# Performance work log

Measured on AMD Instinct MI355X. Metric: run time of the kernel, lower is better.

Reference implementation:

```python
import jax, jax.numpy as jnp
import numpy as np

N, B, NUM_NODES, D_IN = 16384, 16, 1024, 1024
H, C = 4, 128
E = 262144


def _g(k, shape, fan_in):
    return jax.random.normal(k, shape, jnp.float32) * (1.0 / np.sqrt(fan_in))


def setup_inputs() -> dict:
    key = jax.random.key(0)
    ks = jax.random.split(key, 32)
    HC = H * C
    inp = {
        'x': jax.random.normal(ks[0], (N, D_IN), jnp.float32),
        'edge_index': jax.random.randint(ks[1], (2, E), 0, N, dtype=jnp.int64),
        'batch': jnp.repeat(jnp.arange(B, dtype=jnp.int64), NUM_NODES),
        # GATConv 1 (D_IN -> H x C, concat)
        'W1': _g(ks[2], (D_IN, HC), D_IN),
        'att_src1': _g(ks[3], (H, C), C),
        'att_dst1': _g(ks[4], (H, C), C),
        'b1': jnp.zeros((HC,), jnp.float32),
        # GATConv 2 (H*C -> H x C, concat)
        'W2': _g(ks[5], (HC, HC), HC),
        'att_src2': _g(ks[6], (H, C), C),
        'att_dst2': _g(ks[7], (H, C), C),
        'b2': jnp.zeros((HC,), jnp.float32),
        # pooling linears (HC -> 1)
        'p1w': _g(ks[8], (HC, 1), HC), 'p1b': jnp.zeros((1,), jnp.float32),
        'p2w': _g(ks[9], (HC, 1), HC), 'p2b': jnp.zeros((1,), jnp.float32),
        # layer_norm0 (applied to x2 per original code)
        'ln_g': jnp.ones((NUM_NODES,), jnp.float32),
        'ln_b': jnp.zeros((NUM_NODES,), jnp.float32),
        # encoder MLP 1024->512->256->128->64, last 64->1
        'fw1': _g(ks[10], (NUM_NODES, 512), NUM_NODES), 'fb1': jnp.zeros((512,), jnp.float32),
        'fw2': _g(ks[11], (512, 256), 512), 'fb2': jnp.zeros((256,), jnp.float32),
        'fw3': _g(ks[12], (256, 128), 256), 'fb3': jnp.zeros((128,), jnp.float32),
        'fw4': _g(ks[13], (128, 64), 128), 'fb4': jnp.zeros((64,), jnp.float32),
        'lw': _g(ks[14], (64, 1), 64), 'lb': jnp.zeros((1,), jnp.float32),
    }
    return inp


def gat_conv(x, src, dst, W, a_src, a_dst, b):
    # x: [N, F_in] -> h: [N, H, C]
    h = (x @ W).reshape(N, H, C)
    alpha_src = jnp.sum(h * a_src[None], axis=-1)  # [N, H]
    alpha_dst = jnp.sum(h * a_dst[None], axis=-1)  # [N, H]
    e = jax.nn.leaky_relu(alpha_src[src] + alpha_dst[dst], 0.2)  # [E', H]
    # segment softmax over destination neighborhoods (every node has a self loop)
    emax = jax.ops.segment_max(e, dst, num_segments=N)
    ex = jnp.exp(e - emax[dst])
    denom = jax.ops.segment_sum(ex, dst, num_segments=N)
    alpha = ex / (denom[dst] + 1e-16)  # [E', H]
    msg = h[src] * alpha[:, :, None]  # [E', H, C]
    out = jax.ops.segment_sum(msg, dst, num_segments=N)  # [N, H, C]
    return out.reshape(N, H * C) + b


def layer_norm(x, g, b, eps=1e-5):
    mu = jnp.mean(x, axis=-1, keepdims=True)
    var = jnp.var(x, axis=-1, keepdims=True)
    return (x - mu) * jax.lax.rsqrt(var + eps) * g + b


def reference(x, edge_index, batch, W1, att_src1, att_dst1, b1, W2, att_src2, att_dst2, b2,
              p1w, p1b, p2w, p2b, ln_g, ln_b, fw1, fb1, fw2, fb2, fw3, fb3, fw4, fb4, lw, lb):
    # add self loops (GATConv default)
    loops = jnp.arange(N, dtype=edge_index.dtype)
    src = jnp.concatenate([edge_index[0], loops])
    dst = jnp.concatenate([edge_index[1], loops])

    h1 = jax.nn.elu(gat_conv(x, src, dst, W1, att_src1, att_dst1, b1))
    # pool1 + to_dense_batch: batch is sorted with NUM_NODES nodes per graph -> reshape
    x1 = (h1 @ p1w + p1b).squeeze(-1).reshape(B, NUM_NODES)
    h2 = jax.nn.elu(gat_conv(h1, src, dst, W2, att_src2, att_dst2, b2))
    x2 = (h2 @ p2w + p2b).squeeze(-1).reshape(B, NUM_NODES)

    # opt.layer_norm=True; original bug: x2 normalized by layer_norm0
    x2 = layer_norm(x2, ln_g, ln_b)
    multiscale = x2  # which_layer == 'layer3'

    e = jax.nn.elu(multiscale @ fw1 + fb1)
    e = jax.nn.elu(e @ fw2 + fb2)
    e = jax.nn.elu(e @ fw3 + fb3)
    e = jax.nn.elu(e @ fw4 + fb4)
    pred = e @ lw + lb  # act_type='none' -> no activation
    return multiscale, e, pred
```

## Files before the change

kernel.cpp:

```cpp
#include <hip/hip_runtime.h>
#include <math.h>

#define NN    16384
#define DIN   1024
#define HCdim 512
#define NHEAD 4
#define NE_   262144
#define EP_   (NE_ + NN)

using short8  = __attribute__((ext_vector_type(8))) short;
using floatx4 = __attribute__((ext_vector_type(4))) float;

typedef __attribute__((address_space(3))) unsigned int lds_uint;
typedef const __attribute__((address_space(1))) unsigned int glb_uint;
#define ASYNC_LD16(g, l) __builtin_amdgcn_global_load_lds((glb_uint*)(g), (lds_uint*)(l), 16, 0, 0)

__device__ __forceinline__ float eluf(float x){ return x > 0.f ? x : expm1f(x); }
__device__ __forceinline__ float lrelu(float x){ return x > 0.f ? x : 0.2f * x; }
__device__ __forceinline__ float bf2f(unsigned short u){
    union { unsigned int i; float f; } c; c.i = ((unsigned int)u) << 16; return c.f;
}
__device__ __forceinline__ unsigned short f2b(float f){
    union { float f; unsigned int u; } c; c.f = f;
    unsigned int u = c.u;
    return (unsigned short)((u + 0x7FFFu + ((u >> 16) & 1u)) >> 16);
}

__global__ void k_zero_i(int* __restrict__ p, int n){
    int i = blockIdx.x * 256 + threadIdx.x;
    if (i < n) p[i] = 0;
}

__global__ void k_degree(const int* __restrict__ ei, int* __restrict__ deg){
    int i = blockIdx.x * 256 + threadIdx.x;
    if (i >= EP_) return;
    int d = (i < NE_) ? ei[NE_ + i] : (i - NE_);
    atomicAdd(&deg[d], 1);
}

__global__ __launch_bounds__(1024) void k_scan(const int* __restrict__ deg, int* __restrict__ offs){
    __shared__ int s[1024];
    int tid  = threadIdx.x;
    int base = tid * 16;
    int local[16];
    int sum = 0;
    #pragma unroll
    for (int i = 0; i < 16; i++){ local[i] = deg[base + i]; sum += local[i]; }
    s[tid] = sum;
    __syncthreads();
    for (int off = 1; off < 1024; off <<= 1){
        int v = (tid >= off) ? s[tid - off] : 0;
        __syncthreads();
        s[tid] += v;
        __syncthreads();
    }
    int run = (tid == 0) ? 0 : s[tid - 1];
    #pragma unroll
    for (int i = 0; i < 16; i++){ offs[base + i] = run; run += local[i]; }
    if (tid == 1023) offs[NN] = run;
}

__global__ void k_scatter(const int* __restrict__ ei, const int* __restrict__ offs,
                          int* __restrict__ cursor, int* __restrict__ csr){
    int i = blockIdx.x * 256 + threadIdx.x;
    if (i >= EP_) return;
    int srcv, dstv;
    if (i < NE_){ srcv = ei[i]; dstv = ei[NE_ + i]; }
    else        { srcv = dstv = i - NE_; }
    int pos = offs[dstv] + atomicAdd(&cursor[dstv], 1);
    csr[pos] = srcv;
}

__global__ __launch_bounds__(256) void k_casts(const float* __restrict__ x, ushort* __restrict__ xb,
    const float* __restrict__ W1, ushort* __restrict__ W1T,
    const float* __restrict__ W2, ushort* __restrict__ W2T){
    int bid = blockIdx.x, tid = threadIdx.x;
    if (bid < 16384){
        int i = bid * 256 + tid;
        float4 v = *(const float4*)(x + (size_t)i * 4);
        ushort4 o = { f2b(v.x), f2b(v.y), f2b(v.z), f2b(v.w) };
        *(ushort4*)(xb + (size_t)i * 4) = o;
    } else if (bid < 16384 + 512){
        int t = (bid - 16384) * 256 + tid;
        int n = t >> 8, kb = (t & 255) * 4;
        ushort4 o = { f2b(W1[(size_t)(kb+0)*HCdim + n]), f2b(W1[(size_t)(kb+1)*HCdim + n]),
                      f2b(W1[(size_t)(kb+2)*HCdim + n]), f2b(W1[(size_t)(kb+3)*HCdim + n]) };
        *(ushort4*)(W1T + (size_t)n * DIN + kb) = o;
    } else {
        int t = (bid - 16896) * 256 + tid;
        int n = t >> 7, kb = (t & 127) * 4;
        ushort4 o = { f2b(W2[(size_t)(kb+0)*HCdim + n]), f2b(W2[(size_t)(kb+1)*HCdim + n]),
                      f2b(W2[(size_t)(kb+2)*HCdim + n]), f2b(W2[(size_t)(kb+3)*HCdim + n]) };
        *(ushort4*)(W2T + (size_t)n * HCdim + kb) = o;
    }
}

__global__ __launch_bounds__(256) void gemm_bf16(const ushort* __restrict__ A,
                                                 const ushort* __restrict__ BT,
                                                 signed char* __restrict__ C,
                                                 const float* __restrict__ att_s,
                                                 const float* __restrict__ att_d,
                                                 float* __restrict__ as_, float* __restrict__ ad_,
                                                 float* __restrict__ sclb,
                                                 int M, int Nn, int K){
    __shared__ ushort As[2][64 * 32];
    __shared__ ushort Bs[2][128 * 32];
    __shared__ float prS[2][64];
    __shared__ float prD[2][64];
    __shared__ float amx[2][64];
    int tid = threadIdx.x;
    int m0 = blockIdx.x * 64, n0 = blockIdx.y * 128;
    int cx = blockIdx.y;
    int lane = tid & 63, w = tid >> 6;
    int wm = (w >> 1) * 32, wn = (w & 1) * 64;
    int la = lane & 15, qd = lane >> 4;

    int srow = tid >> 2, schunk = (tid & 3) * 8;
    const ushort* Ag = A  + (size_t)(m0 + srow) * K + schunk;
    const ushort* Bg = BT + (size_t)(n0 + srow) * K + schunk;
    ushort* Asw0 = &As[0][srow * 32 + schunk];
    ushort* Asw1 = &As[1][srow * 32 + schunk];
    ushort* Bsw0 = &Bs[0][srow * 32 + schunk];
    ushort* Bsw1 = &Bs[1][srow * 32 + schunk];

    floatx4 acc[4][2] = {};
    for (int k0 = 0; k0 < K; k0 += 64){
        __syncthreads();
        ASYNC_LD16(Ag + k0,                       Asw0);
        ASYNC_LD16(Ag + k0 + 32,                  Asw1);
        ASYNC_LD16(Bg + k0,                       Bsw0);
        ASYNC_LD16(Bg + (size_t)64 * K + k0,      Bsw0 + 64 * 32);
        ASYNC_LD16(Bg + k0 + 32,                  Bsw1);
        ASYNC_LD16(Bg + (size_t)64 * K + k0 + 32, Bsw1 + 64 * 32);
        __syncthreads();
        #pragma unroll
        for (int kk = 0; kk < 2; kk++){
            short8 af[2], bf[4];
            #pragma unroll
            for (int j = 0; j < 2; j++)
                af[j] = *(const short8*)&As[kk][(wm + j*16 + la) * 32 + qd * 8];
            #pragma unroll
            for (int i = 0; i < 4; i++)
                bf[i] = *(const short8*)&Bs[kk][(wn + i*16 + la) * 32 + qd * 8];
            #pragma unroll
            for (int i = 0; i < 4; i++)
                #pragma unroll
                for (int j = 0; j < 2; j++)
                    acc[i][j] = __builtin_amdgcn_mfma_f32_16x16x32_bf16(bf[i], af[j], acc[i][j], 0, 0, 0);
        }
    }
    float4 s4[4], d4[4];
    #pragma unroll
    for (int i = 0; i < 4; i++){
        s4[i] = *(const float4*)(att_s + cx * 128 + wn + i * 16 + qd * 4);
        d4[i] = *(const float4*)(att_d + cx * 128 + wn + i * 16 + qd * 4);
    }
    int half = wn >> 6;
    #pragma unroll
    for (int j = 0; j < 2; j++){
        float ps = 0.f, pd = 0.f;
        #pragma unroll
        for (int i = 0; i < 4; i++){
            ps = fmaf(acc[i][j][0], s4[i].x, ps); pd = fmaf(acc[i][j][0], d4[i].x, pd);
            ps = fmaf(acc[i][j][1], s4[i].y, ps); pd = fmaf(acc[i][j][1], d4[i].y, pd);
            ps = fmaf(acc[i][j][2], s4[i].z, ps); pd = fmaf(acc[i][j][2], d4[i].z, pd);
            ps = fmaf(acc[i][j][3], s4[i].w, ps); pd = fmaf(acc[i][j][3], d4[i].w, pd);
        }
        ps += __shfl_xor(ps, 16); ps += __shfl_xor(ps, 32);
        pd += __shfl_xor(pd, 16); pd += __shfl_xor(pd, 32);
        float am = 0.f;
        #pragma unroll
        for (int i = 0; i < 4; i++){
            am = fmaxf(am, fabsf(acc[i][j][0])); am = fmaxf(am, fabsf(acc[i][j][1]));
            am = fmaxf(am, fabsf(acc[i][j][2])); am = fmaxf(am, fabsf(acc[i][j][3]));
        }
        am = fmaxf(am, __shfl_xor(am, 16)); am = fmaxf(am, __shfl_xor(am, 32));
        if (lane < 16){
            prS[half][wm + j * 16 + la] = ps;
            prD[half][wm + j * 16 + la] = pd;
            amx[half][wm + j * 16 + la] = am;
        }
    }
    __syncthreads();
    #pragma unroll
    for (int j = 0; j < 2; j++){
        int nl = wm + j * 16 + la;
        float amax = fmaxf(fmaxf(amx[0][nl], amx[1][nl]), 1e-20f);
        float inv = 127.0f / amax;
        #pragma unroll
        for (int i = 0; i < 4; i++){
            int q0 = (int)rintf(acc[i][j][0] * inv);
            int q1 = (int)rintf(acc[i][j][1] * inv);
            int q2 = (int)rintf(acc[i][j][2] * inv);
            int q3 = (int)rintf(acc[i][j][3] * inv);
            unsigned pk = (q0 & 0xff) | ((q1 & 0xff) << 8) | ((q2 & 0xff) << 16) | ((q3 & 0xff) << 24);
            *(unsigned*)(C + (size_t)(m0 + nl) * HCdim + n0 + wn + i * 16 + qd * 4) = pk;
        }
    }
    if (tid < 64){
        as_[(size_t)(m0 + tid) * 4 + cx]  = prS[0][tid] + prS[1][tid];
        ad_[(size_t)(m0 + tid) * 4 + cx]  = prD[0][tid] + prD[1][tid];
        sclb[(size_t)(m0 + tid) * 4 + cx] = fmaxf(fmaxf(amx[0][tid], amx[1][tid]), 1e-20f) * (1.f / 127.f);
    }
}

__global__ __launch_bounds__(256) void k_edgew(const int* __restrict__ offs, const int* __restrict__ csr,
    const float* __restrict__ as_, const float* __restrict__ ad_,
    const float* __restrict__ sclb, unsigned* __restrict__ wbuf){
    int wv = threadIdx.x >> 6, lane = threadIdx.x & 63;
    int n = blockIdx.x * 4 + wv;
    int start = offs[n], end = offs[n + 1];
    float4 ad4 = *(const float4*)(ad_ + (size_t)n * 4);
    for (int j = start + lane; j < end; j += 64){
        int s = csr[j];
        float4 as4 = *(const float4*)(as_ + (size_t)s * 4);
        float4 sc4 = *(const float4*)(sclb + (size_t)s * 4);
        float w0 = __expf(lrelu(as4.x + ad4.x));
        float w1 = __expf(lrelu(as4.y + ad4.y));
        float w2 = __expf(lrelu(as4.z + ad4.z));
        float w3 = __expf(lrelu(as4.w + ad4.w));
        uint4 o;
        o.x = (unsigned)f2b(w0) | ((unsigned)f2b(w0 * sc4.x) << 16);
        o.y = (unsigned)f2b(w1) | ((unsigned)f2b(w1 * sc4.y) << 16);
        o.z = (unsigned)f2b(w2) | ((unsigned)f2b(w2 * sc4.z) << 16);
        o.w = (unsigned)f2b(w3) | ((unsigned)f2b(w3 * sc4.w) << 16);
        *(uint4*)(wbuf + (size_t)j * 4) = o;
    }
}

template<bool POOL>
__global__ __launch_bounds__(256) void k_aggregate(const signed char* __restrict__ h,
    const int* __restrict__ offs, const int* __restrict__ csr,
    const unsigned* __restrict__ wbuf,
    const float* __restrict__ bias, ushort* __restrict__ out,
    const float* __restrict__ pw, const float* __restrict__ pb, float* __restrict__ x2){
    int wv   = threadIdx.x >> 6;
    int lane = threadIdx.x & 63;
    int n    = blockIdx.x * 4 + wv;
    int cb   = lane * 8;
    int head = lane >> 4;
    int start = offs[n], end = offs[n + 1];
    const signed char* hrow = h + cb;
    float dsum = 0.f;
    float a0=0.f,a1=0.f,a2=0.f,a3=0.f,a4=0.f,a5=0.f,a6=0.f,a7=0.f;

    for (int base = start; base < end; base += 64){
        int bcnt = min(64, end - base);
        int pre = csr[base + min(lane, bcnt - 1)];
        unsigned wA0, wA1, wA2, wA3, wB0, wB1, wB2, wB3;
        uint2 hA0, hA1, hA2, hA3, hB0, hB1, hB2, hB3;

#define LOADE(W, H, E)                                                        \
        { int e_ = (E); int ec_ = min(e_, bcnt - 1);                          \
          int s_ = __builtin_amdgcn_readlane(pre, ec_);                       \
          unsigned wp_ = wbuf[(size_t)(base + ec_) * 4 + head];               \
          W = (e_ < bcnt) ? wp_ : 0u;                                         \
          H = *(const uint2*)(hrow + (size_t)s_ * HCdim); }

#define CONS(W, H)                                                            \
        { float w_  = bf2f((unsigned short)(W & 0xffff));                     \
          float ws_ = bf2f((unsigned short)(W >> 16));                        \
          dsum += w_;                                                         \
          int q0 = (int)(H.x << 24) >> 24;                                    \
          int q1 = (int)(H.x << 16) >> 24;                                    \
          int q2 = (int)(H.x <<  8) >> 24;                                    \
          int q3 = (int) H.x        >> 24;                                    \
          int q4 = (int)(H.y << 24) >> 24;                                    \
          int q5 = (int)(H.y << 16) >> 24;                                    \
          int q6 = (int)(H.y <<  8) >> 24;                                    \
          int q7 = (int) H.y        >> 24;                                    \
          a0 = fmaf(ws_, (float)q0, a0); a1 = fmaf(ws_, (float)q1, a1);       \
          a2 = fmaf(ws_, (float)q2, a2); a3 = fmaf(ws_, (float)q3, a3);       \
          a4 = fmaf(ws_, (float)q4, a4); a5 = fmaf(ws_, (float)q5, a5);       \
          a6 = fmaf(ws_, (float)q6, a6); a7 = fmaf(ws_, (float)q7, a7); }

        LOADE(wA0, hA0, 0) LOADE(wA1, hA1, 1) LOADE(wA2, hA2, 2) LOADE(wA3, hA3, 3)
        for (int g = 0; g < bcnt; g += 8){
            LOADE(wB0, hB0, g + 4) LOADE(wB1, hB1, g + 5)
            LOADE(wB2, hB2, g + 6) LOADE(wB3, hB3, g + 7)
            CONS(wA0, hA0) CONS(wA1, hA1) CONS(wA2, hA2) CONS(wA3, hA3)
            LOADE(wA0, hA0, g + 8) LOADE(wA1, hA1, g + 9)
            LOADE(wA2, hA2, g + 10) LOADE(wA3, hA3, g + 11)
            CONS(wB0, hB0) CONS(wB1, hB1) CONS(wB2, hB2) CONS(wB3, hB3)
        }
#undef LOADE
#undef CONS
    }
    float rden = 1.f / (dsum + 1e-16f);
    float4 b0 = *(const float4*)(bias + cb);
    float4 b1 = *(const float4*)(bias + cb + 4);
    float e0 = eluf(fmaf(a0, rden, b0.x));
    float e1 = eluf(fmaf(a1, rden, b0.y));
    float e2 = eluf(fmaf(a2, rden, b0.z));
    float e3 = eluf(fmaf(a3, rden, b0.w));
    float e4 = eluf(fmaf(a4, rden, b1.x));
    float e5 = eluf(fmaf(a5, rden, b1.y));
    float e6 = eluf(fmaf(a6, rden, b1.z));
    float e7 = eluf(fmaf(a7, rden, b1.w));
    if (!POOL){
        uint4 o;
        o.x = (unsigned)f2b(e0) | ((unsigned)f2b(e1) << 16);
        o.y = (unsigned)f2b(e2) | ((unsigned)f2b(e3) << 16);
        o.z = (unsigned)f2b(e4) | ((unsigned)f2b(e5) << 16);
        o.w = (unsigned)f2b(e6) | ((unsigned)f2b(e7) << 16);
        *(uint4*)(out + (size_t)n * HCdim + cb) = o;
    } else {
        float4 w0p = *(const float4*)(pw + cb);
        float4 w1p = *(const float4*)(pw + cb + 4);
        float s = e0*w0p.x + e1*w0p.y + e2*w0p.z + e3*w0p.w
                + e4*w1p.x + e5*w1p.y + e6*w1p.z + e7*w1p.w;
        #pragma unroll
        for (int off = 32; off; off >>= 1) s += __shfl_down(s, off);
        if (lane == 0) x2[n] = s + pb[0];
    }
}

__global__ __launch_bounds__(256) void k_fc1_ln(const float* __restrict__ x2,
    const float* __restrict__ lng, const float* __restrict__ lnb,
    const float* __restrict__ W, const float* __restrict__ bias,
    float* __restrict__ outms, float* __restrict__ e1b){
    __shared__ float xs[1024];
    __shared__ float red[4][64];
    __shared__ float red2[8];
    __shared__ float stats[2];
    int tid = threadIdx.x;
    int b = blockIdx.y, c0 = blockIdx.x * 64;
    float4 v = *(const float4*)(x2 + b * 1024 + tid * 4);
    float s  = v.x + v.y + v.z + v.w;
    float sq = v.x * v.x + v.y * v.y + v.z * v.z + v.w * v.w;
    #pragma unroll
    for (int off = 32; off; off >>= 1){ s += __shfl_down(s, off); sq += __shfl_down(sq, off); }
    if ((tid & 63) == 0){ red2[(tid >> 6) * 2] = s; red2[(tid >> 6) * 2 + 1] = sq; }
    __syncthreads();
    if (tid == 0){
        float S  = red2[0] + red2[2] + red2[4] + red2[6];
        float SQ = red2[1] + red2[3] + red2[5] + red2[7];
        float mu  = S * (1.f / 1024.f);
        float var = SQ * (1.f / 1024.f) - mu * mu;
        stats[0] = mu; stats[1] = rsqrtf(var + 1e-5f);
    }
    __syncthreads();
    float mu = stats[0], r = stats[1];
    float4 g4  = *(const float4*)(lng + tid * 4);
    float4 bb4 = *(const float4*)(lnb + tid * 4);
    float4 o;
    o.x = (v.x - mu) * r * g4.x + bb4.x;
    o.y = (v.y - mu) * r * g4.y + bb4.y;
    o.z = (v.z - mu) * r * g4.z + bb4.z;
    o.w = (v.w - mu) * r * g4.w + bb4.w;
    *(float4*)&xs[tid * 4] = o;
    if (blockIdx.x == 0) *(float4*)(outms + b * 1024 + tid * 4) = o;
    __syncthreads();
    int tx = tid & 63, ty = tid >> 6;
    const float* wp = W + (size_t)(ty * 256) * 512 + c0 + tx;
    float a = 0.f;
    #pragma unroll 8
    for (int i = 0; i < 256; i++)
        a = fmaf(xs[ty * 256 + i], wp[(size_t)i * 512], a);
    red[ty][tx] = a;
    __syncthreads();
    if (ty == 0){
        float vv = red[0][tx] + red[1][tx] + red[2][tx] + red[3][tx] + bias[c0 + tx];
        e1b[b * 512 + c0 + tx] = eluf(vv);
    }
}

template<int K, int NOUT>
__global__ __launch_bounds__(256) void k_fc(const float* __restrict__ in,
    const float* __restrict__ W, const float* __restrict__ bias, float* __restrict__ outb){
    __shared__ float xs[K];
    __shared__ float red[4][64];
    int tid = threadIdx.x;
    int b = blockIdx.y, c0 = blockIdx.x * 64;
    int tx = tid & 63, ty = tid >> 6;
    for (int i = tid * 4; i < K; i += 1024)
        *(float4*)&xs[i] = *(const float4*)(in + b * K + i);
    __syncthreads();
    const float* wp = W + (size_t)(ty * (K / 4)) * NOUT + c0 + tx;
    float a = 0.f;
    #pragma unroll 8
    for (int i = 0; i < K / 4; i++)
        a = fmaf(xs[ty * (K / 4) + i], wp[(size_t)i * NOUT], a);
    red[ty][tx] = a;
    __syncthreads();
    if (ty == 0){
        float v = red[0][tx] + red[1][tx] + red[2][tx] + red[3][tx] + bias[c0 + tx];
        outb[b * NOUT + tx + c0] = eluf(v);
    }
}

__global__ __launch_bounds__(256) void k_fc_final(const float* __restrict__ in,
    const float* __restrict__ W, const float* __restrict__ bias,
    const float* __restrict__ lw, const float* __restrict__ lb, float* __restrict__ out){
    __shared__ float xs[128];
    __shared__ float red[4][64];
    __shared__ float evs[64];
    int tid = threadIdx.x;
    int b = blockIdx.x;
    int tx = tid & 63, ty = tid >> 6;
    if (tid * 4 < 128)
        *(float4*)&xs[tid * 4] = *(const float4*)(in + b * 128 + tid * 4);
    __syncthreads();
    const float* wp = W + (size_t)(ty * 32) * 64 + tx;
    float a = 0.f;
    #pragma unroll
    for (int i = 0; i < 32; i++)
        a = fmaf(xs[ty * 32 + i], wp[(size_t)i * 64], a);
    red[ty][tx] = a;
    __syncthreads();
    if (ty == 0){
        float ev = eluf(red[0][tx] + red[1][tx] + red[2][tx] + red[3][tx] + bias[tx]);
        evs[tx] = ev;
        out[16384 + b * 64 + tx] = ev;
    }
    __syncthreads();
    if (ty == 0){
        float p = evs[tx] * lw[tx];
        #pragma unroll
        for (int off = 32; off; off >>= 1) p += __shfl_down(p, off);
        if (tx == 0) out[16384 + 1024 + b] = p + lb[0];
    }
}

extern "C" void kernel_launch(void* const* d_in, const int* in_sizes, int n_in,
                              void* d_out, int out_size, void* d_ws, size_t ws_size,
                              hipStream_t stream) {
    const float* x        = (const float*)d_in[0];
    const int*   ei       = (const int*)  d_in[1];
    const float* W1       = (const float*)d_in[3];
    const float* att_src1 = (const float*)d_in[4];
    const float* att_dst1 = (const float*)d_in[5];
    const float* b1       = (const float*)d_in[6];
    const float* W2       = (const float*)d_in[7];
    const float* att_src2 = (const float*)d_in[8];
    const float* att_dst2 = (const float*)d_in[9];
    const float* b2       = (const float*)d_in[10];
    const float* p2w      = (const float*)d_in[13];
    const float* p2b      = (const float*)d_in[14];
    const float* ln_g     = (const float*)d_in[15];
    const float* ln_b     = (const float*)d_in[16];
    const float* fw1      = (const float*)d_in[17];
    const float* fb1      = (const float*)d_in[18];
    const float* fw2      = (const float*)d_in[19];
    const float* fb2      = (const float*)d_in[20];
    const float* fw3      = (const float*)d_in[21];
    const float* fb3      = (const float*)d_in[22];
    const float* fw4      = (const float*)d_in[23];
    const float* fb4      = (const float*)d_in[24];
    const float* lw       = (const float*)d_in[25];
    const float* lb       = (const float*)d_in[26];
    float* out = (float*)d_out;

    char* w = (char*)d_ws;
    ushort* xb   = (ushort*)(w);
    ushort* h1b  = (ushort*)(w);
    signed char* hpre = (signed char*)(w + 33554432);
    ushort* W1T  = (ushort*)(w + 41943040);
    ushort* W2T  = (ushort*)(w + 42991616);
    float* asb   = (float*)(w + 43515904);
    float* adb   = (float*)(w + 43778048);
    float* sclb  = (float*)(w + 44040192);
    int*   deg   = (int*)  (w + 44302336);
    int*   cursor= (int*)  (w + 44367872);
    int*   offs  = (int*)  (w + 44433408);
    int*   csr   = (int*)  (w + 44499200);
    unsigned* wbuf = (unsigned*)(w + 45613312);
    float* x2b   = (float*)(w + 50069760);
    float* e1b   = (float*)(w + 50135296);
    float* e2b   = (float*)(w + 50167808);
    float* e3b   = (float*)(w + 50184192);

    k_zero_i <<<(2 * NN + 255) / 256, 256, 0, stream>>>(deg, 2 * NN);
    k_degree <<<(EP_ + 255) / 256, 256, 0, stream>>>(ei, deg);
    k_scan   <<<1, 1024, 0, stream>>>(deg, offs);
    k_scatter<<<(EP_ + 255) / 256, 256, 0, stream>>>(ei, offs, cursor, csr);

    k_casts<<<16384 + 512 + 256, 256, 0, stream>>>(x, xb, W1, W1T, W2, W2T);

    dim3 ggrid(NN / 64, HCdim / 128);
    gemm_bf16         <<<ggrid, 256, 0, stream>>>(xb, W1T, hpre, att_src1, att_dst1,
                                                  asb, adb, sclb, NN, HCdim, DIN);
    k_edgew           <<<NN / 4, 256, 0, stream>>>(offs, csr, asb, adb, sclb, wbuf);
    k_aggregate<false><<<NN / 4, 256, 0, stream>>>(hpre, offs, csr, wbuf, b1, h1b,
                                                   nullptr, nullptr, nullptr);
    gemm_bf16         <<<ggrid, 256, 0, stream>>>(h1b, W2T, hpre, att_src2, att_dst2,
                                                  asb, adb, sclb, NN, HCdim, HCdim);
    k_edgew           <<<NN / 4, 256, 0, stream>>>(offs, csr, asb, adb, sclb, wbuf);
    k_aggregate<true> <<<NN / 4, 256, 0, stream>>>(hpre, offs, csr, wbuf, b2, nullptr,
                                                   p2w, p2b, x2b);
    k_fc1_ln          <<<dim3(8, 16), 256, 0, stream>>>(x2b, ln_g, ln_b, fw1, fb1, out, e1b);
    k_fc< 512, 256>   <<<dim3(4, 16), 256, 0, stream>>>(e1b, fw2, fb2, e2b);
    k_fc< 256, 128>   <<<dim3(2, 16), 256, 0, stream>>>(e2b, fw3, fb3, e3b);
    k_fc_final        <<<16, 256, 0, stream>>>(e3b, fw4, fb4, lw, lb, out);
}
```

Baseline: 347.8 us.

## Split aggregation channels across two waves per node to double parallelism

Each destination node's 512 channels are now handled by two wavefronts, each covering half the channels with 4-byte loads instead of 8-byte loads, and the grid is doubled. The pooled variant combines the two partial dot products with atomicAdd into a pre-zeroed buffer, and the pooling bias moves into the layer-norm kernel. The aim is more waves in flight to hide gather latency. In exchange, edge indices and weights are re-read by both waves, each load is narrower, and an extra zeroing launch plus atomics are added.

```diff
diff --git a/kernel.cpp b/kernel.cpp
--- a/kernel.cpp
+++ b/kernel.cpp
@@ -233,89 +233,79 @@
     const int* __restrict__ offs, const int* __restrict__ csr,
     const unsigned* __restrict__ wbuf,
     const float* __restrict__ bias, ushort* __restrict__ out,
-    const float* __restrict__ pw, const float* __restrict__ pb, float* __restrict__ x2){
-    int wv   = threadIdx.x >> 6;
-    int lane = threadIdx.x & 63;
-    int n    = blockIdx.x * 4 + wv;
-    int cb   = lane * 8;
-    int head = lane >> 4;
+    const float* __restrict__ pw, float* __restrict__ x2){
+    int tid  = threadIdx.x;
+    int wv   = tid >> 6;
+    int lane = tid & 63;
+    int g    = blockIdx.x;
+    int r    = g & 7;
+    int half = r >> 2;
+    int n    = (g >> 3) * 16 + (r & 3) * 4 + wv;
+    int cb   = half * 256 + lane * 4;
+    int head = cb >> 7;
     int start = offs[n], end = offs[n + 1];
     const signed char* hrow = h + cb;
     float dsum = 0.f;
-    float a0=0.f,a1=0.f,a2=0.f,a3=0.f,a4=0.f,a5=0.f,a6=0.f,a7=0.f;
+    float a0 = 0.f, a1 = 0.f, a2 = 0.f, a3 = 0.f;
 
     for (int base = start; base < end; base += 64){
         int bcnt = min(64, end - base);
         int pre = csr[base + min(lane, bcnt - 1)];
         unsigned wA0, wA1, wA2, wA3, wB0, wB1, wB2, wB3;
-        uint2 hA0, hA1, hA2, hA3, hB0, hB1, hB2, hB3;
+        unsigned hA0, hA1, hA2, hA3, hB0, hB1, hB2, hB3;
 
 #define LOADE(W, H, E)                                                        \
         { int e_ = (E); int ec_ = min(e_, bcnt - 1);                          \
           int s_ = __builtin_amdgcn_readlane(pre, ec_);                       \
           unsigned wp_ = wbuf[(size_t)(base + ec_) * 4 + head];               \
           W = (e_ < bcnt) ? wp_ : 0u;                                         \
-          H = *(const uint2*)(hrow + (size_t)s_ * HCdim); }
+          H = *(const unsigned*)(hrow + (size_t)s_ * HCdim); }
 
 #define CONS(W, H)                                                            \
         { float w_  = bf2f((unsigned short)(W & 0xffff));                     \
           float ws_ = bf2f((unsigned short)(W >> 16));                        \
           dsum += w_;                                                         \
-          int q0 = (int)(H.x << 24) >> 24;                                    \
-          int q1 = (int)(H.x << 16) >> 24;                                    \
-          int q2 = (int)(H.x <<  8) >> 24;                                    \
-          int q3 = (int) H.x        >> 24;                                    \
-          int q4 = (int)(H.y << 24) >> 24;                                    \
-          int q5 = (int)(H.y << 16) >> 24;                                    \
-          int q6 = (int)(H.y <<  8) >> 24;                                    \
-          int q7 = (int) H.y        >> 24;                                    \
+          int q0 = (int)(H << 24) >> 24;                                      \
+          int q1 = (int)(H << 16) >> 24;                                      \
+          int q2 = (int)(H <<  8) >> 24;                                      \
+          int q3 = (int) H        >> 24;                                      \
           a0 = fmaf(ws_, (float)q0, a0); a1 = fmaf(ws_, (float)q1, a1);       \
-          a2 = fmaf(ws_, (float)q2, a2); a3 = fmaf(ws_, (float)q3, a3);       \
-          a4 = fmaf(ws_, (float)q4, a4); a5 = fmaf(ws_, (float)q5, a5);       \
-          a6 = fmaf(ws_, (float)q6, a6); a7 = fmaf(ws_, (float)q7, a7); }
+          a2 = fmaf(ws_, (float)q2, a2); a3 = fmaf(ws_, (float)q3, a3); }
 
         LOADE(wA0, hA0, 0) LOADE(wA1, hA1, 1) LOADE(wA2, hA2, 2) LOADE(wA3, hA3, 3)
-        for (int g = 0; g < bcnt; g += 8){
-            LOADE(wB0, hB0, g + 4) LOADE(wB1, hB1, g + 5)
-            LOADE(wB2, hB2, g + 6) LOADE(wB3, hB3, g + 7)
+        for (int gg = 0; gg < bcnt; gg += 8){
+            LOADE(wB0, hB0, gg + 4) LOADE(wB1, hB1, gg + 5)
+            LOADE(wB2, hB2, gg + 6) LOADE(wB3, hB3, gg + 7)
             CONS(wA0, hA0) CONS(wA1, hA1) CONS(wA2, hA2) CONS(wA3, hA3)
-            LOADE(wA0, hA0, g + 8) LOADE(wA1, hA1, g + 9)
-            LOADE(wA2, hA2, g + 10) LOADE(wA3, hA3, g + 11)
+            LOADE(wA0, hA0, gg + 8) LOADE(wA1, hA1, gg + 9)
+            LOADE(wA2, hA2, gg + 10) LOADE(wA3, hA3, gg + 11)
             CONS(wB0, hB0) CONS(wB1, hB1) CONS(wB2, hB2) CONS(wB3, hB3)
         }
 #undef LOADE
 #undef CONS
     }
     float rden = 1.f / (dsum + 1e-16f);
-    float4 b0 = *(const float4*)(bias + cb);
-    float4 b1 = *(const float4*)(bias + cb + 4);
-    float e0 = eluf(fmaf(a0, rden, b0.x));
-    float e1 = eluf(fmaf(a1, rden, b0.y));
-    float e2 = eluf(fmaf(a2, rden, b0.z));
-    float e3 = eluf(fmaf(a3, rden, b0.w));
-    float e4 = eluf(fmaf(a4, rden, b1.x));
-    float e5 = eluf(fmaf(a5, rden, b1.y));
-    float e6 = eluf(fmaf(a6, rden, b1.z));
-    float e7 = eluf(fmaf(a7, rden, b1.w));
+    float4 b4 = *(const float4*)(bias + cb);
+    float e0 = eluf(fmaf(a0, rden, b4.x));
+    float e1 = eluf(fmaf(a1, rden, b4.y));
+    float e2 = eluf(fmaf(a2, rden, b4.z));
+    float e3 = eluf(fmaf(a3, rden, b4.w));
     if (!POOL){
-        uint4 o;
+        uint2 o;
         o.x = (unsigned)f2b(e0) | ((unsigned)f2b(e1) << 16);
         o.y = (unsigned)f2b(e2) | ((unsigned)f2b(e3) << 16);
-        o.z = (unsigned)f2b(e4) | ((unsigned)f2b(e5) << 16);
-        o.w = (unsigned)f2b(e6) | ((unsigned)f2b(e7) << 16);
-        *(uint4*)(out + (size_t)n * HCdim + cb) = o;
+        *(uint2*)(out + (size_t)n * HCdim + cb) = o;
     } else {
-        float4 w0p = *(const float4*)(pw + cb);
-        float4 w1p = *(const float4*)(pw + cb + 4);
-        float s = e0*w0p.x + e1*w0p.y + e2*w0p.z + e3*w0p.w
-                + e4*w1p.x + e5*w1p.y + e6*w1p.z + e7*w1p.w;
+        float4 w4 = *(const float4*)(pw + cb);
+        float s = e0 * w4.x + e1 * w4.y + e2 * w4.z + e3 * w4.w;
         #pragma unroll
         for (int off = 32; off; off >>= 1) s += __shfl_down(s, off);
-        if (lane == 0) x2[n] = s + pb[0];
+        if (lane == 0) atomicAdd(&x2[n], s);
     }
 }
 
 __global__ __launch_bounds__(256) void k_fc1_ln(const float* __restrict__ x2,
+    const float* __restrict__ pb,
     const float* __restrict__ lng, const float* __restrict__ lnb,
     const float* __restrict__ W, const float* __restrict__ bias,
     float* __restrict__ outms, float* __restrict__ e1b){
@@ -325,7 +315,9 @@
     __shared__ float stats[2];
     int tid = threadIdx.x;
     int b = blockIdx.y, c0 = blockIdx.x * 64;
+    float pbv = pb[0];
     float4 v = *(const float4*)(x2 + b * 1024 + tid * 4);
+    v.x += pbv; v.y += pbv; v.z += pbv; v.w += pbv;
     float s  = v.x + v.y + v.z + v.w;
     float sq = v.x * v.x + v.y * v.y + v.z * v.z + v.w * v.w;
     #pragma unroll
@@ -471,6 +463,7 @@
     float* e3b   = (float*)(w + 50184192);
 
     k_zero_i <<<(2 * NN + 255) / 256, 256, 0, stream>>>(deg, 2 * NN);
+    k_zero_i <<<(NN + 255) / 256, 256, 0, stream>>>((int*)x2b, NN);
     k_degree <<<(EP_ + 255) / 256, 256, 0, stream>>>(ei, deg);
     k_scan   <<<1, 1024, 0, stream>>>(deg, offs);
     k_scatter<<<(EP_ + 255) / 256, 256, 0, stream>>>(ei, offs, cursor, csr);
@@ -481,14 +474,14 @@
     gemm_bf16         <<<ggrid, 256, 0, stream>>>(xb, W1T, hpre, att_src1, att_dst1,
                                                   asb, adb, sclb, NN, HCdim, DIN);
     k_edgew           <<<NN / 4, 256, 0, stream>>>(offs, csr, asb, adb, sclb, wbuf);
-    k_aggregate<false><<<NN / 4, 256, 0, stream>>>(hpre, offs, csr, wbuf, b1, h1b,
-                                                   nullptr, nullptr, nullptr);
+    k_aggregate<false><<<NN / 2, 256, 0, stream>>>(hpre, offs, csr, wbuf, b1, h1b,
+                                                   nullptr, nullptr);
     gemm_bf16         <<<ggrid, 256, 0, stream>>>(h1b, W2T, hpre, att_src2, att_dst2,
                                                   asb, adb, sclb, NN, HCdim, HCdim);
     k_edgew           <<<NN / 4, 256, 0, stream>>>(offs, csr, asb, adb, sclb, wbuf);
-    k_aggregate<true> <<<NN / 4, 256, 0, stream>>>(hpre, offs, csr, wbuf, b2, nullptr,
-                                                   p2w, p2b, x2b);
-    k_fc1_ln          <<<dim3(8, 16), 256, 0, stream>>>(x2b, ln_g, ln_b, fw1, fb1, out, e1b);
+    k_aggregate<true> <<<NN / 2, 256, 0, stream>>>(hpre, offs, csr, wbuf, b2, nullptr,
+                                                   p2w, x2b);
+    k_fc1_ln          <<<dim3(8, 16), 256, 0, stream>>>(x2b, p2b, ln_g, ln_b, fw1, fb1, out, e1b);
     k_fc< 512, 256>   <<<dim3(4, 16), 256, 0, stream>>>(e1b, fw2, fb2, e2b);
     k_fc< 256, 128>   <<<dim3(2, 16), 256, 0, stream>>>(e2b, fw3, fb3, e3b);
     k_fc_final        <<<16, 256, 0, stream>>>(e3b, fw4, fb4, lw, lb, out);
```

Result: slower. 356.7 us (+2.6%).
